# Optimization experiments

Measured on AMD Instinct MI355X. Metric: run time of the kernel, lower is better.

## Reference

```python
import jax, jax.numpy as jnp
import numpy as np

N_NODES = 50000
N_EDGES = 800000
IN_DIM = 128
HIDDEN = 128
LN_EPS = 1e-5


def setup_inputs() -> dict:
    key = jax.random.key(0)
    ks = jax.random.split(key, 10)
    x = jax.random.normal(ks[0], (N_NODES, IN_DIM), dtype=jnp.float32)
    edge_index = jax.random.randint(ks[1], (2, N_EDGES), 0, N_NODES, dtype=jnp.int32)
    # GCNConv linear weights (glorot-ish) + bias, per layer
    W1 = jax.random.normal(ks[2], (IN_DIM, HIDDEN), dtype=jnp.float32) / np.sqrt(IN_DIM)
    b1 = jnp.zeros((HIDDEN,), dtype=jnp.float32)
    W2 = jax.random.normal(ks[3], (HIDDEN, HIDDEN), dtype=jnp.float32) / np.sqrt(HIDDEN)
    b2 = jnp.zeros((HIDDEN,), dtype=jnp.float32)
    # LayerNorm affine params per layer
    g1 = jnp.ones((HIDDEN,), dtype=jnp.float32)
    beta1 = jnp.zeros((HIDDEN,), dtype=jnp.float32)
    g2 = jnp.ones((HIDDEN,), dtype=jnp.float32)
    beta2 = jnp.zeros((HIDDEN,), dtype=jnp.float32)
    return {"x": x, "edge_index": edge_index, "W1": W1, "b1": b1,
            "g1": g1, "beta1": beta1, "W2": W2, "b2": b2,
            "g2": g2, "beta2": beta2}


def _gcn_layer(h, W, b, src, dst):
    # h: [N, Din] -> [N, Dout]; src/dst: [E] (source j -> target i)
    n = h.shape[0]
    h = h @ W
    loops = jnp.arange(n, dtype=src.dtype)
    s = jnp.concatenate([src, loops])  # [E+N]
    d = jnp.concatenate([dst, loops])
    deg = jax.ops.segment_sum(jnp.ones(s.shape[0], dtype=h.dtype), d, num_segments=n)
    dinv = jnp.where(deg > 0, jax.lax.rsqrt(jnp.maximum(deg, 1.0)), 0.0)
    norm = dinv[s] * dinv[d]  # [E+N] symmetric normalization
    out = jax.ops.segment_sum(h[s] * norm[:, None], d, num_segments=n)
    return out + b


def _layer_norm(h, g, b):
    mu = jnp.mean(h, axis=-1, keepdims=True)
    var = jnp.mean(jnp.square(h - mu), axis=-1, keepdims=True)
    return (h - mu) * jax.lax.rsqrt(var + LN_EPS) * g + b


def reference(x, edge_index, W1, b1, g1, beta1, W2, b2, g2, beta2):
    src, dst = edge_index[0], edge_index[1]
    h = _gcn_layer(x, W1, b1, src, dst)
    h = jax.nn.relu(_layer_norm(h, g1, beta1))
    h = _gcn_layer(h, W2, b2, src, dst)
    h = jax.nn.relu(_layer_norm(h, g2, beta2))
    return h
```

## Files before the change

kernel.cpp:

```cpp
#include <hip/hip_runtime.h>

#define LN_EPS 1e-5f

typedef __attribute__((ext_vector_type(8))) short bf16x8;
typedef __attribute__((ext_vector_type(4))) float f32x4;

#define BSH 7
#define BSPAN 128
#define BCAP 4096
#define BIN_TILE 4096

__device__ __forceinline__ unsigned short f2bf(float f) {
    union { float f; unsigned u; } x; x.f = f;
    unsigned r = (x.u + 0x7FFFu + ((x.u >> 16) & 1u)) >> 16;
    return (unsigned short)r;
}
__device__ __forceinline__ float bfbits2f(unsigned hi) {
    union { unsigned u; float f; } x; x.u = hi; return x.f;
}

__global__ void convx_k(const float* __restrict__ X, unsigned short* __restrict__ Xb,
                        int total, int total_pad) {
    int i = blockIdx.x * blockDim.x + threadIdx.x;
    if (i < total_pad) Xb[i] = (i < total) ? f2bf(X[i]) : (unsigned short)0;
}

__global__ void packw_k(const float* __restrict__ W1, const float* __restrict__ W2,
                        unsigned short* __restrict__ Wp1, unsigned short* __restrict__ Wp2,
                        int* __restrict__ gcur, int nb) {
    int idx = blockIdx.x * blockDim.x + threadIdx.x;
    if (blockIdx.x == 0) {
        for (int i = threadIdx.x; i < nb; i += 256) gcur[i] = 0;
    }
    const float* W = (idx < 16384) ? W1 : W2;
    unsigned short* Wp = (idx < 16384) ? Wp1 : Wp2;
    int t = idx & 16383;
    int k = t >> 7, col = t & 127;
    int kc = k >> 5, kr = k & 31, kb = kr >> 3, j = kr & 7;
    Wp[(((kc * 128 + col) * 4 + kb) * 8) + j] = f2bf(W[k * 128 + col]);
}

__global__ __launch_bounds__(256) void bin_k(const int* __restrict__ src,
                                             const int* __restrict__ dst,
                                             int* __restrict__ gcur,
                                             unsigned* __restrict__ staging,
                                             int nE, int nb) {
    __shared__ int cnt[512];
    __shared__ int gbase[512];
    int tid = threadIdx.x;
    for (int i = tid; i < nb; i += 256) cnt[i] = 0;
    __syncthreads();
    int e0 = blockIdx.x * BIN_TILE;
    unsigned pk[16];
    int bk[16];
    int rk[16];
#pragma unroll
    for (int i = 0; i < 16; ++i) {
        int e = e0 + i * 256 + tid;
        if (e < nE) {
            int s = src[e];
            int d = dst[e];
            int b = d >> BSH;
            rk[i] = atomicAdd(&cnt[b], 1);
            bk[i] = b;
            pk[i] = (unsigned)s | ((unsigned)(d & (BSPAN - 1)) << 17);
        } else {
            bk[i] = -1;
        }
    }
    __syncthreads();
    for (int i = tid; i < nb; i += 256) gbase[i] = atomicAdd(&gcur[i], cnt[i]);
    __syncthreads();
#pragma unroll
    for (int i = 0; i < 16; ++i) {
        if (bk[i] >= 0)
            staging[(size_t)bk[i] * BCAP + gbase[bk[i]] + rk[i]] = pk[i];
    }
}

__global__ __launch_bounds__(512) void bscan_k(const int* __restrict__ gcur,
                                               int* __restrict__ bbase,
                                               int* __restrict__ rowptr,
                                               int n, int nb, int nE) {
    __shared__ int s[512];
    int tid = threadIdx.x;
    int v = (tid < nb) ? gcur[tid] : 0;
    s[tid] = v;
    __syncthreads();
    for (int off = 1; off < 512; off <<= 1) {
        int t = (tid >= off) ? s[tid - off] : 0;
        __syncthreads();
        s[tid] += t;
        __syncthreads();
    }
    if (tid < nb) bbase[tid] = s[tid] - v;
    if (tid == nb - 1) { bbase[nb] = s[tid]; rowptr[n] = nE; }
}

__global__ __launch_bounds__(256) void build_k(const unsigned* __restrict__ staging,
                                               const int* __restrict__ bbase,
                                               int* __restrict__ rowptr,
                                               int* __restrict__ eidx,
                                               float* __restrict__ dinv, int n) {
    __shared__ int cnt[BSPAN];
    __shared__ int off[BSPAN];
    __shared__ int s[BSPAN];
    int b = blockIdx.x;
    int tid = threadIdx.x;
    if (tid < BSPAN) cnt[tid] = 0;
    __syncthreads();
    int base = bbase[b];
    int total = bbase[b + 1] - base;
    const unsigned* stg = staging + (size_t)b * BCAP;
    unsigned ent[16];
#pragma unroll
    for (int k = 0; k < 16; ++k) {
        int i = tid + k * 256;
        unsigned e = 0xFFFFFFFFu;
        if (i < total) {
            e = stg[i];
            atomicAdd(&cnt[(e >> 17) & (BSPAN - 1)], 1);
        }
        ent[k] = e;
    }
    __syncthreads();
    if (tid < BSPAN) s[tid] = cnt[tid];
    __syncthreads();
    for (int o = 1; o < BSPAN; o <<= 1) {
        int t = (tid < BSPAN && tid >= o) ? s[tid - o] : 0;
        __syncthreads();
        if (tid < BSPAN) s[tid] += t;
        __syncthreads();
    }
    if (tid < BSPAN) {
        int excl = s[tid] - cnt[tid];
        off[tid] = excl;
        int node = b * BSPAN + tid;
        if (node < n) {
            rowptr[node] = base + excl;
            dinv[node] = rsqrtf((float)(cnt[tid] + 1));
        }
    }
    __syncthreads();
#pragma unroll
    for (int k = 0; k < 16; ++k) {
        unsigned e = ent[k];
        if (e != 0xFFFFFFFFu) {
            int ld = (e >> 17) & (BSPAN - 1);
            int p = atomicAdd(&off[ld], 1);
            eidx[base + p] = (int)(e & 0x1FFFFu);
        }
    }
}

__global__ __launch_bounds__(256) void mfma_gemm_k(const unsigned short* __restrict__ Xb,
                                                   const unsigned short* __restrict__ Wp,
                                                   const float* __restrict__ dinv,
                                                   unsigned short* __restrict__ Y, int n) {
    int wid = threadIdx.x >> 6;
    int lane = threadIdx.x & 63;
    int rgrp = wid & 1;
    int cgrp = wid >> 1;
    int row0 = blockIdx.x * 64 + rgrp * 32;
    int m = lane & 15;
    int kb = lane >> 4;

    f32x4 acc[2][4] = {};
#pragma unroll
    for (int kc = 0; kc < 4; ++kc) {
        bf16x8 a[2], b[4];
#pragma unroll
        for (int rs = 0; rs < 2; ++rs) {
            int r = row0 + rs * 16 + m;
            a[rs] = *(const bf16x8*)(Xb + (size_t)r * 128 + kc * 32 + kb * 8);
        }
#pragma unroll
        for (int cf = 0; cf < 4; ++cf) {
            int col = cgrp * 64 + cf * 16 + m;
            b[cf] = *(const bf16x8*)(Wp + (((kc * 128 + col) * 4 + kb) * 8));
        }
#pragma unroll
        for (int rs = 0; rs < 2; ++rs)
#pragma unroll
            for (int cf = 0; cf < 4; ++cf)
                acc[rs][cf] = __builtin_amdgcn_mfma_f32_16x16x32_bf16(a[rs], b[cf], acc[rs][cf], 0, 0, 0);
    }
#pragma unroll
    for (int rs = 0; rs < 2; ++rs) {
        int rbase = row0 + rs * 16 + kb * 4;
#pragma unroll
        for (int r = 0; r < 4; ++r) {
            int row = rbase + r;
            if (row >= n) continue;
            float dv = dinv[row];
#pragma unroll
            for (int cf = 0; cf < 4; ++cf) {
                int col = cgrp * 64 + cf * 16 + m;
                Y[(size_t)row * 128 + col] = f2bf(acc[rs][cf][r] * dv);
            }
        }
    }
}

#define ACCU(u) { \
    a0 += bfbits2f((u).x << 16); a1 += bfbits2f((u).x & 0xFFFF0000u); \
    a2 += bfbits2f((u).y << 16); a3 += bfbits2f((u).y & 0xFFFF0000u); \
    a4 += bfbits2f((u).z << 16); a5 += bfbits2f((u).z & 0xFFFF0000u); \
    a6 += bfbits2f((u).w << 16); a7 += bfbits2f((u).w & 0xFFFF0000u); }

template <bool OUT_BF16>
__global__ __launch_bounds__(256) void agg_ln_k(const unsigned short* __restrict__ Hs,
                                                const float* __restrict__ dinv,
                                                const int* __restrict__ rowptr,
                                                const int* __restrict__ eidx,
                                                const float* __restrict__ bias,
                                                const float* __restrict__ g,
                                                const float* __restrict__ beta,
                                                void* __restrict__ out, int n) {
    int wave = (blockIdx.x * blockDim.x + threadIdx.x) >> 6;
    int lane = threadIdx.x & 63;
    if (wave >= n) return;
    int q = lane & 15;
    int grp = lane >> 4;
    const uint4* H16 = (const uint4*)Hs;

    float a0 = 0.f, a1 = 0.f, a2 = 0.f, a3 = 0.f, a4 = 0.f, a5 = 0.f, a6 = 0.f, a7 = 0.f;
    if (grp == 0) {
        uint4 sv = H16[(size_t)wave * 16 + q];
        ACCU(sv);
    }
    int beg = rowptr[wave];
    int end = rowptr[wave + 1];
    int eb = beg;
    for (; eb + 7 < end; eb += 8) {
        int s0 = eidx[eb + grp];
        int s1 = eidx[eb + 4 + grp];
        uint4 u0 = H16[(size_t)s0 * 16 + q];
        uint4 u1 = H16[(size_t)s1 * 16 + q];
        ACCU(u0);
        ACCU(u1);
    }
    {
        int e0 = eb + grp;
        int e1 = eb + 4 + grp;
        if (e0 < end) { uint4 u = H16[(size_t)eidx[e0] * 16 + q]; ACCU(u); }
        if (e1 < end) { uint4 u = H16[(size_t)eidx[e1] * 16 + q]; ACCU(u); }
    }
    a0 += __shfl_xor(a0, 16); a1 += __shfl_xor(a1, 16);
    a2 += __shfl_xor(a2, 16); a3 += __shfl_xor(a3, 16);
    a4 += __shfl_xor(a4, 16); a5 += __shfl_xor(a5, 16);
    a6 += __shfl_xor(a6, 16); a7 += __shfl_xor(a7, 16);
    a0 += __shfl_xor(a0, 32); a1 += __shfl_xor(a1, 32);
    a2 += __shfl_xor(a2, 32); a3 += __shfl_xor(a3, 32);
    a4 += __shfl_xor(a4, 32); a5 += __shfl_xor(a5, 32);
    a6 += __shfl_xor(a6, 32); a7 += __shfl_xor(a7, 32);

    float dt = dinv[wave];
    float4 bi0 = ((const float4*)bias)[2 * q];
    float4 bi1 = ((const float4*)bias)[2 * q + 1];
    float v0 = a0 * dt + bi0.x, v1 = a1 * dt + bi0.y;
    float v2 = a2 * dt + bi0.z, v3 = a3 * dt + bi0.w;
    float v4 = a4 * dt + bi1.x, v5 = a5 * dt + bi1.y;
    float v6 = a6 * dt + bi1.z, v7 = a7 * dt + bi1.w;

    float sum = ((v0 + v1) + (v2 + v3)) + ((v4 + v5) + (v6 + v7));
    sum += __shfl_xor(sum, 1);
    sum += __shfl_xor(sum, 2);
    sum += __shfl_xor(sum, 4);
    sum += __shfl_xor(sum, 8);
    float mu = sum * (1.0f / 128.0f);
    float d0 = v0 - mu, d1 = v1 - mu, d2 = v2 - mu, d3 = v3 - mu;
    float d4 = v4 - mu, d5 = v5 - mu, d6 = v6 - mu, d7 = v7 - mu;
    float vs = ((d0 * d0 + d1 * d1) + (d2 * d2 + d3 * d3)) +
               ((d4 * d4 + d5 * d5) + (d6 * d6 + d7 * d7));
    vs += __shfl_xor(vs, 1);
    vs += __shfl_xor(vs, 2);
    vs += __shfl_xor(vs, 4);
    vs += __shfl_xor(vs, 8);
    float rstd = rsqrtf(vs * (1.0f / 128.0f) + LN_EPS);

    float4 gg0 = ((const float4*)g)[2 * q];
    float4 gg1 = ((const float4*)g)[2 * q + 1];
    float4 bb0 = ((const float4*)beta)[2 * q];
    float4 bb1 = ((const float4*)beta)[2 * q + 1];
    float o0 = fmaxf(d0 * rstd * gg0.x + bb0.x, 0.0f);
    float o1 = fmaxf(d1 * rstd * gg0.y + bb0.y, 0.0f);
    float o2 = fmaxf(d2 * rstd * gg0.z + bb0.z, 0.0f);
    float o3 = fmaxf(d3 * rstd * gg0.w + bb0.w, 0.0f);
    float o4 = fmaxf(d4 * rstd * gg1.x + bb1.x, 0.0f);
    float o5 = fmaxf(d5 * rstd * gg1.y + bb1.y, 0.0f);
    float o6 = fmaxf(d6 * rstd * gg1.z + bb1.z, 0.0f);
    float o7 = fmaxf(d7 * rstd * gg1.w + bb1.w, 0.0f);

    if (grp == 0) {
        if (OUT_BF16) {
            uint4 pk;
            pk.x = (unsigned)f2bf(o0) | ((unsigned)f2bf(o1) << 16);
            pk.y = (unsigned)f2bf(o2) | ((unsigned)f2bf(o3) << 16);
            pk.z = (unsigned)f2bf(o4) | ((unsigned)f2bf(o5) << 16);
            pk.w = (unsigned)f2bf(o6) | ((unsigned)f2bf(o7) << 16);
            ((uint4*)out)[(size_t)wave * 16 + q] = pk;
        } else {
            float4* o = (float4*)out;
            o[(size_t)wave * 32 + 2 * q]     = make_float4(o0, o1, o2, o3);
            o[(size_t)wave * 32 + 2 * q + 1] = make_float4(o4, o5, o6, o7);
        }
    }
}

extern "C" void kernel_launch(void* const* d_in, const int* in_sizes, int n_in,
                              void* d_out, int out_size, void* d_ws, size_t ws_size,
                              hipStream_t stream) {
    const float* x   = (const float*)d_in[0];
    const int*   ei  = (const int*)d_in[1];
    const float* W1  = (const float*)d_in[2];
    const float* b1  = (const float*)d_in[3];
    const float* g1  = (const float*)d_in[4];
    const float* be1 = (const float*)d_in[5];
    const float* W2  = (const float*)d_in[6];
    const float* b2  = (const float*)d_in[7];
    const float* g2  = (const float*)d_in[8];
    const float* be2 = (const float*)d_in[9];
    float* out = (float*)d_out;

    int n  = in_sizes[0] / 128;
    int nE = in_sizes[1] / 2;
    const int* src = ei;
    const int* dst = ei + nE;

    int nb = (n + BSPAN - 1) >> BSH;
    int nblk64 = (n + 63) / 64;
    int npad   = nblk64 * 64;

    char* p = (char*)d_ws;
    auto carve = [&](size_t bytes) {
        char* r = p;
        p += (bytes + 255) & ~(size_t)255;
        return r;
    };
    float*    dinv    = (float*)carve((size_t)n * 4);
    int*      rowptr  = (int*)carve((size_t)(n + 1) * 4);
    int*      eidx    = (int*)carve((size_t)nE * 4);
    int*      gcur    = (int*)carve((size_t)nb * 4);
    int*      bbase   = (int*)carve((size_t)(nb + 1) * 4);
    unsigned* staging = (unsigned*)carve((size_t)nb * BCAP * 4);
    unsigned short* Wp1 = (unsigned short*)carve(16384 * 2);
    unsigned short* Wp2 = (unsigned short*)carve(16384 * 2);
    unsigned short* Xb  = (unsigned short*)carve((size_t)npad * 128 * 2);
    unsigned short* Hs  = (unsigned short*)carve((size_t)npad * 128 * 2);
    unsigned short* Hb  = (unsigned short*)carve((size_t)npad * 128 * 2);

    dim3 blk(256);
    int total = n * 128, total_pad = npad * 128;
    int nbin = (nE + BIN_TILE - 1) / BIN_TILE;

    packw_k<<<32768 / 256, blk, 0, stream>>>(W1, W2, Wp1, Wp2, gcur, nb);
    convx_k<<<(total_pad + 255) / 256, blk, 0, stream>>>(x, Xb, total, total_pad);

    bin_k<<<nbin, blk, 0, stream>>>(src, dst, gcur, staging, nE, nb);
    bscan_k<<<1, dim3(512), 0, stream>>>(gcur, bbase, rowptr, n, nb, nE);
    build_k<<<nb, blk, 0, stream>>>(staging, bbase, rowptr, eidx, dinv, n);

    int nwave_blocks = (n + 3) / 4;

    mfma_gemm_k<<<nblk64, blk, 0, stream>>>(Xb, Wp1, dinv, Hs, n);
    agg_ln_k<true><<<nwave_blocks, blk, 0, stream>>>(Hs, dinv, rowptr, eidx, b1, g1, be1, Hb, n);

    mfma_gemm_k<<<nblk64, blk, 0, stream>>>(Hb, Wp2, dinv, Hs, n);
    agg_ln_k<false><<<nwave_blocks, blk, 0, stream>>>(Hs, dinv, rowptr, eidx, b2, g2, be2, out, n);
}
```

Baseline: 229.7 us.

## Fuse x conversion into GEMM, drop bucket scan kernel, software-pipeline gathers

Removes the standalone fp32-to-bf16 conversion kernel by having the first GEMM load fp32 rows and pack them to bf16 with v_cvt_pk_bf16_f32. Removes the single-block bucket scan kernel, so each build block now computes its own base offset by summing the preceding bucket counts. The aggregation loop is restructured to prefetch the next batch of neighbour rows before accumulating the current one, which overlaps gather latency with compute. Together these cut two launches and one full pass over x, at the cost of redundant prefix sums in every build block and higher register use in the aggregation kernel.

```diff
diff --git a/kernel.cpp b/kernel.cpp
--- a/kernel.cpp
+++ b/kernel.cpp
@@ -18,11 +18,10 @@
 __device__ __forceinline__ float bfbits2f(unsigned hi) {
     union { unsigned u; float f; } x; x.u = hi; return x.f;
 }
-
-__global__ void convx_k(const float* __restrict__ X, unsigned short* __restrict__ Xb,
-                        int total, int total_pad) {
-    int i = blockIdx.x * blockDim.x + threadIdx.x;
-    if (i < total_pad) Xb[i] = (i < total) ? f2bf(X[i]) : (unsigned short)0;
+__device__ __forceinline__ unsigned cvtpk_bf16(float lo, float hi) {
+    unsigned r;
+    asm("v_cvt_pk_bf16_f32 %0, %1, %2" : "=v"(r) : "v"(lo), "v"(hi));
+    return r;
 }
 
 __global__ void packw_k(const float* __restrict__ W1, const float* __restrict__ W2,
@@ -78,39 +77,28 @@
     }
 }
 
-__global__ __launch_bounds__(512) void bscan_k(const int* __restrict__ gcur,
-                                               int* __restrict__ bbase,
-                                               int* __restrict__ rowptr,
-                                               int n, int nb, int nE) {
-    __shared__ int s[512];
-    int tid = threadIdx.x;
-    int v = (tid < nb) ? gcur[tid] : 0;
-    s[tid] = v;
-    __syncthreads();
-    for (int off = 1; off < 512; off <<= 1) {
-        int t = (tid >= off) ? s[tid - off] : 0;
-        __syncthreads();
-        s[tid] += t;
-        __syncthreads();
-    }
-    if (tid < nb) bbase[tid] = s[tid] - v;
-    if (tid == nb - 1) { bbase[nb] = s[tid]; rowptr[n] = nE; }
-}
-
 __global__ __launch_bounds__(256) void build_k(const unsigned* __restrict__ staging,
-                                               const int* __restrict__ bbase,
+                                               const int* __restrict__ gcur,
                                                int* __restrict__ rowptr,
                                                int* __restrict__ eidx,
-                                               float* __restrict__ dinv, int n) {
+                                               float* __restrict__ dinv, int n, int nE) {
     __shared__ int cnt[BSPAN];
     __shared__ int off[BSPAN];
     __shared__ int s[BSPAN];
+    __shared__ int red[4];
     int b = blockIdx.x;
     int tid = threadIdx.x;
     if (tid < BSPAN) cnt[tid] = 0;
-    __syncthreads();
-    int base = bbase[b];
-    int total = bbase[b + 1] - base;
+    int part = 0;
+    for (int i = tid; i < b; i += 256) part += gcur[i];
+#pragma unroll
+    for (int o = 32; o > 0; o >>= 1) part += __shfl_down(part, o);
+    if ((tid & 63) == 0) red[tid >> 6] = part;
+    __syncthreads();
+    int base = red[0] + red[1] + red[2] + red[3];
+    int total = gcur[b];
+    if (b == 0 && tid == 0) rowptr[n] = nE;
+
     const unsigned* stg = staging + (size_t)b * BCAP;
     unsigned ent[16];
 #pragma unroll
@@ -153,7 +141,8 @@
     }
 }
 
-__global__ __launch_bounds__(256) void mfma_gemm_k(const unsigned short* __restrict__ Xb,
+template <bool A_F32>
+__global__ __launch_bounds__(256) void mfma_gemm_k(const void* __restrict__ Ain,
                                                    const unsigned short* __restrict__ Wp,
                                                    const float* __restrict__ dinv,
                                                    unsigned short* __restrict__ Y, int n) {
@@ -172,7 +161,21 @@
 #pragma unroll
         for (int rs = 0; rs < 2; ++rs) {
             int r = row0 + rs * 16 + m;
-            a[rs] = *(const bf16x8*)(Xb + (size_t)r * 128 + kc * 32 + kb * 8);
+            if (A_F32) {
+                f32x4 f0 = {0.f, 0.f, 0.f, 0.f}, f1 = {0.f, 0.f, 0.f, 0.f};
+                if (r < n) {
+                    const float* ap = (const float*)Ain + (size_t)r * 128 + kc * 32 + kb * 8;
+                    f0 = *(const f32x4*)ap;
+                    f1 = *(const f32x4*)(ap + 4);
+                }
+                unsigned* w = (unsigned*)&a[rs];
+                w[0] = cvtpk_bf16(f0.x, f0.y);
+                w[1] = cvtpk_bf16(f0.z, f0.w);
+                w[2] = cvtpk_bf16(f1.x, f1.y);
+                w[3] = cvtpk_bf16(f1.z, f1.w);
+            } else {
+                a[rs] = *(const bf16x8*)((const unsigned short*)Ain + (size_t)r * 128 + kc * 32 + kb * 8);
+            }
         }
 #pragma unroll
         for (int cf = 0; cf < 4; ++cf) {
@@ -224,27 +227,44 @@
     int grp = lane >> 4;
     const uint4* H16 = (const uint4*)Hs;
 
+    int beg = rowptr[wave];
+    int end = rowptr[wave + 1];
+    float dt = dinv[wave];
+
     float a0 = 0.f, a1 = 0.f, a2 = 0.f, a3 = 0.f, a4 = 0.f, a5 = 0.f, a6 = 0.f, a7 = 0.f;
     if (grp == 0) {
         uint4 sv = H16[(size_t)wave * 16 + q];
         ACCU(sv);
     }
-    int beg = rowptr[wave];
-    int end = rowptr[wave + 1];
-    int eb = beg;
-    for (; eb + 7 < end; eb += 8) {
-        int s0 = eidx[eb + grp];
-        int s1 = eidx[eb + 4 + grp];
-        uint4 u0 = H16[(size_t)s0 * 16 + q];
-        uint4 u1 = H16[(size_t)s1 * 16 + q];
-        ACCU(u0);
-        ACCU(u1);
-    }
-    {
-        int e0 = eb + grp;
-        int e1 = eb + 4 + grp;
-        if (e0 < end) { uint4 u = H16[(size_t)eidx[e0] * 16 + q]; ACCU(u); }
-        if (e1 < end) { uint4 u = H16[(size_t)eidx[e1] * 16 + q]; ACCU(u); }
+    if (beg < end) {
+        bool p0, p1;
+        uint4 u0, u1;
+        {
+            int e0 = beg + grp, e1 = beg + 4 + grp;
+            p0 = e0 < end; p1 = e1 < end;
+            int i0 = wave, i1 = wave;
+            if (p0) i0 = eidx[e0];
+            if (p1) i1 = eidx[e1];
+            u0 = H16[(size_t)i0 * 16 + q];
+            u1 = H16[(size_t)i1 * 16 + q];
+        }
+        for (int eb = beg + 8;; eb += 8) {
+            bool c0 = p0, c1 = p1;
+            uint4 v0 = u0, v1 = u1;
+            bool more = eb < end;
+            if (more) {
+                int e0 = eb + grp, e1 = eb + 4 + grp;
+                p0 = e0 < end; p1 = e1 < end;
+                int i0 = wave, i1 = wave;
+                if (p0) i0 = eidx[e0];
+                if (p1) i1 = eidx[e1];
+                u0 = H16[(size_t)i0 * 16 + q];
+                u1 = H16[(size_t)i1 * 16 + q];
+            }
+            if (c0) ACCU(v0);
+            if (c1) ACCU(v1);
+            if (!more) break;
+        }
     }
     a0 += __shfl_xor(a0, 16); a1 += __shfl_xor(a1, 16);
     a2 += __shfl_xor(a2, 16); a3 += __shfl_xor(a3, 16);
@@ -255,7 +275,6 @@
     a4 += __shfl_xor(a4, 32); a5 += __shfl_xor(a5, 32);
     a6 += __shfl_xor(a6, 32); a7 += __shfl_xor(a7, 32);
 
-    float dt = dinv[wave];
     float4 bi0 = ((const float4*)bias)[2 * q];
     float4 bi1 = ((const float4*)bias)[2 * q + 1];
     float v0 = a0 * dt + bi0.x, v1 = a1 * dt + bi0.y;
@@ -342,30 +361,24 @@
     int*      rowptr  = (int*)carve((size_t)(n + 1) * 4);
     int*      eidx    = (int*)carve((size_t)nE * 4);
     int*      gcur    = (int*)carve((size_t)nb * 4);
-    int*      bbase   = (int*)carve((size_t)(nb + 1) * 4);
     unsigned* staging = (unsigned*)carve((size_t)nb * BCAP * 4);
     unsigned short* Wp1 = (unsigned short*)carve(16384 * 2);
     unsigned short* Wp2 = (unsigned short*)carve(16384 * 2);
-    unsigned short* Xb  = (unsigned short*)carve((size_t)npad * 128 * 2);
     unsigned short* Hs  = (unsigned short*)carve((size_t)npad * 128 * 2);
     unsigned short* Hb  = (unsigned short*)carve((size_t)npad * 128 * 2);
 
     dim3 blk(256);
-    int total = n * 128, total_pad = npad * 128;
     int nbin = (nE + BIN_TILE - 1) / BIN_TILE;
+    int nwave_blocks = (n + 3) / 4;
 
     packw_k<<<32768 / 256, blk, 0, stream>>>(W1, W2, Wp1, Wp2, gcur, nb);
-    convx_k<<<(total_pad + 255) / 256, blk, 0, stream>>>(x, Xb, total, total_pad);
 
     bin_k<<<nbin, blk, 0, stream>>>(src, dst, gcur, staging, nE, nb);
-    bscan_k<<<1, dim3(512), 0, stream>>>(gcur, bbase, rowptr, n, nb, nE);
-    build_k<<<nb, blk, 0, stream>>>(staging, bbase, rowptr, eidx, dinv, n);
-
-    int nwave_blocks = (n + 3) / 4;
-
-    mfma_gemm_k<<<nblk64, blk, 0, stream>>>(Xb, Wp1, dinv, Hs, n);
+    build_k<<<nb, blk, 0, stream>>>(staging, gcur, rowptr, eidx, dinv, n, nE);
+
+    mfma_gemm_k<true><<<nblk64, blk, 0, stream>>>(x, Wp1, dinv, Hs, n);
     agg_ln_k<true><<<nwave_blocks, blk, 0, stream>>>(Hs, dinv, rowptr, eidx, b1, g1, be1, Hb, n);
 
-    mfma_gemm_k<<<nblk64, blk, 0, stream>>>(Hb, Wp2, dinv, Hs, n);
+    mfma_gemm_k<false><<<nblk64, blk, 0, stream>>>(Hb, Wp2, dinv, Hs, n);
     agg_ln_k<false><<<nwave_blocks, blk, 0, stream>>>(Hs, dinv, rowptr, eidx, b2, g2, be2, out, n);
 }
```

New measurement: 218.2 us. -5.0%, faster.
